# Optimization experiments

Hardware: AMD Instinct MI355X
Metric: run time of the kernel (lower is better)

The kernel has to match this reference:

```python
import jax, jax.numpy as jnp
import numpy as np

HIDDEN = 1024
NUM_HEADS = 4
HEAD_DIM = HIDDEN // NUM_HEADS
SCALE = HEAD_DIM ** -0.5
EPS = 1e-5


def setup_inputs() -> dict:
    key = jax.random.key(0)
    ks = jax.random.split(key, 8)
    B, S, D = 4, 2048, HIDDEN
    x = jax.random.normal(ks[0], (B, S, D), dtype=jnp.float32)
    attention_mask = jnp.ones((B, S), dtype=jnp.int32)
    init = 1.0 / np.sqrt(D)
    Wq = jax.random.uniform(ks[1], (D, D), jnp.float32, -init, init)
    Wk = jax.random.uniform(ks[2], (D, D), jnp.float32, -init, init)
    Wv = jax.random.uniform(ks[3], (D, D), jnp.float32, -init, init)
    Wo = jax.random.uniform(ks[4], (D, D), jnp.float32, -init, init)
    bo = jax.random.uniform(ks[5], (D,), jnp.float32, -init, init)
    gamma = jnp.ones((D,), dtype=jnp.float32)
    beta = jnp.zeros((D,), dtype=jnp.float32)
    return {"x": x, "attention_mask": attention_mask, "Wq": Wq, "Wk": Wk,
            "Wv": Wv, "Wo": Wo, "bo": bo, "gamma": gamma, "beta": beta}


def reference(x, attention_mask, Wq, Wk, Wv, Wo, bo, gamma, beta):
    # Linear layers: y = x @ W^T (torch nn.Linear convention), no bias for q/k/v
    q = jnp.einsum('bsd,ed->bse', x, Wq)
    k = jnp.einsum('bsd,ed->bse', x, Wk)
    v = jnp.einsum('bsd,ed->bse', x, Wv)
    # Full-width attention (module never splits heads), scale = head_dim^-0.5
    scores = jnp.einsum('bqd,bkd->bqk', q, k) * SCALE  # [B,S,S]
    mask = attention_mask[:, None, :]  # [B,1,S]
    scores = jnp.where(mask == 0, jnp.float32(-1e9), scores)
    attn = jax.nn.softmax(scores, axis=-1)
    ctx = jnp.einsum('bqk,bkd->bqd', attn, v)
    out = jnp.einsum('bsd,ed->bse', ctx, Wo) + bo
    # residual + LayerNorm
    h = out + x
    mu = jnp.mean(h, axis=-1, keepdims=True)
    var = jnp.mean(jnp.square(h - mu), axis=-1, keepdims=True)
    return (h - mu) * jax.lax.rsqrt(var + EPS) * gamma + beta
```

## Files before the change

kernel.cpp:

```cpp
#include <hip/hip_runtime.h>

typedef __bf16 bf16;
typedef __bf16 bf16x8 __attribute__((ext_vector_type(8)));
typedef __bf16 bf16x4 __attribute__((ext_vector_type(4)));
typedef float floatx4 __attribute__((ext_vector_type(4)));

#define HIDDEN 1024
#define SEQ 2048
#define BATCH 4
#define ATT_SCALE 0.0625f
#define LN_EPS 1e-5f
#define WW (HIDDEN * HIDDEN)

__device__ __forceinline__ void gload_lds16(const void* g, void* l) {
    __builtin_amdgcn_global_load_lds(
        (const __attribute__((address_space(1))) unsigned int*)g,
        (__attribute__((address_space(3))) unsigned int*)l, 16, 0, 0);
}

#define GBAR() asm volatile("s_barrier" ::: "memory")
#define MFMA(a, b, c) __builtin_amdgcn_mfma_f32_16x16x32_bf16(a, b, c, 0, 0, 0)

__global__ void cvt_f32_bf16(const float* __restrict__ in, bf16* __restrict__ out, int n4) {
    int i = blockIdx.x * blockDim.x + threadIdx.x;
    if (i >= n4) return;
    float4 v = ((const float4*)in)[i];
    bf16x4 o;
    o[0] = (bf16)v.x; o[1] = (bf16)v.y; o[2] = (bf16)v.z; o[3] = (bf16)v.w;
    ((bf16x4*)out)[i] = o;
}

__global__ void transpose_w3(const float* __restrict__ s0, const float* __restrict__ s1,
                             const float* __restrict__ s2,
                             bf16* __restrict__ d0p, bf16* __restrict__ d1p, bf16* __restrict__ d2p) {
    const float* in = (blockIdx.z == 0) ? s0 : (blockIdx.z == 1) ? s1 : s2;
    bf16* out = (blockIdx.z == 0) ? d0p : (blockIdx.z == 1) ? d1p : d2p;
    __shared__ __attribute__((aligned(16))) bf16 tile[64][72];
    const int d0 = blockIdx.x * 64;
    const int f0 = blockIdx.y * 64;
    const int t = threadIdx.x;
    const int r = t >> 4;
    const int c = (t & 15) * 4;
#pragma unroll
    for (int i = 0; i < 4; ++i) {
        float4 v = *(const float4*)&in[(long)(f0 + r + i * 16) * HIDDEN + d0 + c];
        bf16x4 b;
        b[0] = (bf16)v.x; b[1] = (bf16)v.y; b[2] = (bf16)v.z; b[3] = (bf16)v.w;
        *(bf16x4*)&tile[r + i * 16][c] = b;
    }
    __syncthreads();
#pragma unroll
    for (int i = 0; i < 4; ++i) {
        const int dr = r + i * 16;
        bf16x4 o;
#pragma unroll
        for (int j = 0; j < 4; ++j) o[j] = tile[c + j][dr];
        *(bf16x4*)&out[(long)(d0 + dr) * HIDDEN + f0 + c] = o;
    }
}

template <int BNv, int MODE>
__global__ __launch_bounds__(512, 2)
void gemm256(const bf16* A, const bf16* Bw, void* __restrict__ Cout,
             int lda, int ldb, int ldc, int K, float scale,
             long sA, long sB, long sC, int zmod) {
    constexpr int ABY = 256 * 128;
    constexpr int BBY = BNv * 128;
    constexpr int SLOT = ABY + BBY;
    constexpr int AU = ABY / 8192;
    constexpr int BU = BBY / 8192;
    constexpr int WNc = (BNv == 256) ? 4 : 2;
    constexpr int MR = (BNv == 256) ? 8 : 4;
    constexpr int MH = MR / 2;

    __shared__ __attribute__((aligned(16))) char lds[2 * SLOT];

    const int gx = gridDim.x;
    const int nblk = gx * gridDim.y;
    const int bid = blockIdx.y * gx + blockIdx.x;
    const int cpx = nblk >> 3;
    const int sbid = (nblk & 7) ? bid : (bid & 7) * cpx + (bid >> 3);
    const int bx = sbid % gx, by = sbid / gx;

    const int z = blockIdx.z;
    const int mat = z % zmod, ks = z / zmod;
    const char* Ab = (const char*)(A + (long)mat * sA + (long)ks * K);
    const char* Bb = (const char*)(Bw + (long)mat * sB + (long)ks * K);
    const long lda2 = lda * 2L, ldb2 = ldb * 2L;

    const int t = threadIdx.x;
    const int lane = t & 63;
    const int w = t >> 6;
    const int wm = w / WNc, wn = w % WNc;
    const int l15 = lane & 15;
    const int l4 = lane >> 4;

    const int row0 = by * 256;
    const int col0 = bx * BNv;

    const int srow = t >> 3;
    const int soff = (((t & 7) - (srow & 7)) & 7) * 16;
    const char* aP = Ab + (long)(row0 + srow) * lda2 + soff;
    const char* bP = Bb + (long)(col0 + srow) * ldb2 + soff;
    const int ld16 = t * 16;

    auto STAGE = [&](int slot, long koff) {
        char* base = &lds[slot * SLOT];
#pragma unroll
        for (int u = 0; u < AU; ++u)
            gload_lds16(aP + u * 64 * lda2 + koff, base + u * 8192 + ld16);
#pragma unroll
        for (int u = 0; u < BU; ++u)
            gload_lds16(bP + u * 64 * ldb2 + koff, base + ABY + u * 8192 + ld16);
    };

    floatx4 acc[MR][4] = {};
    const int nk = K / 64;

    STAGE(0, 0);
    asm volatile("s_waitcnt vmcnt(0)" ::: "memory");
    GBAR();

    for (int tt = 0; tt < nk; ++tt) {
        const char* sb = &lds[(tt & 1) * SLOT];

        auto RDA = [&](int m, int kkh) {
            int lr = wm * (MR * 16) + m * 16 + l15;
            return *(const bf16x8*)(sb + lr * 128 + (((kkh * 4 + l4 + lr) & 7) << 4));
        };
        auto RDB = [&](int n, int kkh) {
            int lr = wn * 64 + n * 16 + l15;
            return *(const bf16x8*)(sb + ABY + lr * 128 + (((kkh * 4 + l4 + lr) & 7) << 4));
        };

        bf16x8 alo[MH][2], ahi[MH][2], b0[2][2], b1[2][2];
#pragma unroll
        for (int m = 0; m < MH; ++m) { alo[m][0] = RDA(m, 0); alo[m][1] = RDA(m, 1); }
#pragma unroll
        for (int n = 0; n < 2; ++n) {
            b0[n][0] = RDB(n, 0); b0[n][1] = RDB(n, 1);
            b1[n][0] = RDB(2 + n, 0); b1[n][1] = RDB(2 + n, 1);
        }

        if (tt + 1 < nk) STAGE((tt + 1) & 1, (long)(tt + 1) * 128);

        __builtin_amdgcn_s_setprio(1);
#pragma unroll
        for (int m = 0; m < MH; ++m)
#pragma unroll
            for (int n = 0; n < 2; ++n) {
                acc[m][n] = MFMA(alo[m][0], b0[n][0], acc[m][n]);
                acc[m][n] = MFMA(alo[m][1], b0[n][1], acc[m][n]);
            }
        __builtin_amdgcn_s_setprio(0);

#pragma unroll
        for (int m = 0; m < MH; ++m) { ahi[m][0] = RDA(MH + m, 0); ahi[m][1] = RDA(MH + m, 1); }

        __builtin_amdgcn_s_setprio(1);
#pragma unroll
        for (int m = 0; m < MH; ++m)
#pragma unroll
            for (int n = 0; n < 2; ++n) {
                acc[m][2 + n] = MFMA(alo[m][0], b1[n][0], acc[m][2 + n]);
                acc[m][2 + n] = MFMA(alo[m][1], b1[n][1], acc[m][2 + n]);
            }
#pragma unroll
        for (int m = 0; m < MH; ++m)
#pragma unroll
            for (int n = 0; n < 2; ++n) {
                acc[MH + m][n] = MFMA(ahi[m][0], b0[n][0], acc[MH + m][n]);
                acc[MH + m][n] = MFMA(ahi[m][1], b0[n][1], acc[MH + m][n]);
            }
#pragma unroll
        for (int m = 0; m < MH; ++m)
#pragma unroll
            for (int n = 0; n < 2; ++n) {
                acc[MH + m][2 + n] = MFMA(ahi[m][0], b1[n][0], acc[MH + m][2 + n]);
                acc[MH + m][2 + n] = MFMA(ahi[m][1], b1[n][1], acc[MH + m][2 + n]);
            }
        __builtin_amdgcn_s_setprio(0);

        asm volatile("s_waitcnt vmcnt(0)" ::: "memory");
        GBAR();
    }

    const int rq = l4 * 4;
    if constexpr (MODE == 0) {
        bf16* C = ((bf16*)Cout) + (long)z * sC;
#pragma unroll
        for (int m = 0; m < MR; ++m)
#pragma unroll
            for (int i = 0; i < 4; ++i) {
                long gr = row0 + wm * (MR * 16) + m * 16 + rq + i;
#pragma unroll
                for (int n = 0; n < 4; ++n) {
                    int gc = col0 + wn * 64 + n * 16 + l15;
                    C[gr * ldc + gc] = (bf16)(acc[m][n][i] * scale);
                }
            }
    } else {
        float* C = (float*)Cout + (long)z * sC;
#pragma unroll
        for (int m = 0; m < MR; ++m)
#pragma unroll
            for (int i = 0; i < 4; ++i) {
                long gr = row0 + wm * (MR * 16) + m * 16 + rq + i;
#pragma unroll
                for (int n = 0; n < 4; ++n) {
                    int gc = col0 + wn * 64 + n * 16 + l15;
                    C[gr * ldc + gc] = acc[m][n][i];
                }
            }
    }
}

__global__ void reduce_wgc(const float* __restrict__ p, bf16* __restrict__ out) {
    int i = blockIdx.x * blockDim.x + threadIdx.x;
    int e = i * 4;
    int mat = e >> 20;
    int local = e & (WW - 1);
    float4 s = *(const float4*)(p + (long)mat * WW + local);
#pragma unroll
    for (int ksp = 1; ksp < 4; ++ksp) {
        float4 a = *(const float4*)(p + (long)(ksp * 2 + mat) * WW + local);
        s.x += a.x; s.y += a.y; s.z += a.z; s.w += a.w;
    }
    bf16x4 o;
    o[0] = (bf16)s.x; o[1] = (bf16)s.y; o[2] = (bf16)s.z; o[3] = (bf16)s.w;
    *(bf16x4*)&out[e] = o;
}

__global__ void softmax_rows(bf16* __restrict__ S, const int* __restrict__ mask) {
    const int b = blockIdx.y;
    const int row = blockIdx.x;
    bf16* srow = S + ((long)b * SEQ + row) * SEQ;
    const int* mrow = mask + b * SEQ;
    const int t = threadIdx.x;

    bf16x8 sv = *(const bf16x8*)&srow[t * 8];
    int4 m0 = ((const int4*)mrow)[t * 2];
    int4 m1 = ((const int4*)mrow)[t * 2 + 1];
    int mk[8] = {m0.x, m0.y, m0.z, m0.w, m1.x, m1.y, m1.z, m1.w};

    float v[8];
    float mx = -1e30f;
#pragma unroll
    for (int j = 0; j < 8; ++j) {
        float s = (float)sv[j];
        if (mk[j] == 0) s = -1e9f;
        v[j] = s;
        mx = fmaxf(mx, s);
    }
    __shared__ float redm[4], reds[4];
#pragma unroll
    for (int off = 32; off > 0; off >>= 1) mx = fmaxf(mx, __shfl_down(mx, off));
    if ((t & 63) == 0) redm[t >> 6] = mx;
    __syncthreads();
    mx = fmaxf(fmaxf(redm[0], redm[1]), fmaxf(redm[2], redm[3]));

    float sum = 0.f;
#pragma unroll
    for (int j = 0; j < 8; ++j) {
        v[j] = __expf(v[j] - mx);
        sum += v[j];
    }
#pragma unroll
    for (int off = 32; off > 0; off >>= 1) sum += __shfl_down(sum, off);
    if ((t & 63) == 0) reds[t >> 6] = sum;
    __syncthreads();
    sum = reds[0] + reds[1] + reds[2] + reds[3];
    float inv = 1.0f / sum;

    bf16x8 o;
#pragma unroll
    for (int j = 0; j < 8; ++j) o[j] = (bf16)(v[j] * inv);
    *(bf16x8*)&srow[t * 8] = o;
}

__global__ void transpose_v(const bf16* __restrict__ yv, bf16* __restrict__ out) {
    __shared__ __attribute__((aligned(16))) bf16 tile[64][72];
    const int z = blockIdx.z;
    const bf16* ib = yv + (long)z * SEQ * 2048 + 1024;
    bf16* ob = out + (long)z * SEQ * HIDDEN;
    const int d0 = blockIdx.x * 64;
    const int s0 = blockIdx.y * 64;
    const int t = threadIdx.x;
    const int r = t >> 4;
    const int c = (t & 15) * 4;
#pragma unroll
    for (int i = 0; i < 4; ++i) {
        bf16x4 v = *(const bf16x4*)&ib[(long)(s0 + r + i * 16) * 2048 + d0 + c];
        *(bf16x4*)&tile[r + i * 16][c] = v;
    }
    __syncthreads();
#pragma unroll
    for (int i = 0; i < 4; ++i) {
        const int dr = r + i * 16;
        bf16x4 o;
#pragma unroll
        for (int j = 0; j < 4; ++j) o[j] = tile[c + j][dr];
        *(bf16x4*)&ob[(long)(d0 + dr) * SEQ + s0 + c] = o;
    }
}

__global__ void layernorm_out(const bf16* __restrict__ pp, const float* __restrict__ x,
                              const float* __restrict__ bo, const float* __restrict__ gamma,
                              const float* __restrict__ beta, float* __restrict__ out) {
    const long row = blockIdx.x;
    const int b = (int)(row >> 11);
    const int s = (int)(row & 2047);
    const bf16* r0 = pp + ((long)b * SEQ + s) * HIDDEN;
    const bf16* r1 = r0 + 4L * SEQ * HIDDEN;
    const int t = threadIdx.x;

    bf16x4 a0 = ((const bf16x4*)r0)[t];
    bf16x4 a1 = ((const bf16x4*)r1)[t];
    float4 xv = ((const float4*)(x + row * HIDDEN))[t];
    float4 bv = ((const float4*)bo)[t];
    float4 v;
    v.x = (float)a0[0] + (float)a1[0] + bv.x + xv.x;
    v.y = (float)a0[1] + (float)a1[1] + bv.y + xv.y;
    v.z = (float)a0[2] + (float)a1[2] + bv.z + xv.z;
    v.w = (float)a0[3] + (float)a1[3] + bv.w + xv.w;

    float ssum = v.x + v.y + v.z + v.w;
    float sq = v.x * v.x + v.y * v.y + v.z * v.z + v.w * v.w;
    __shared__ float rs[4], rq[4];
#pragma unroll
    for (int off = 32; off > 0; off >>= 1) {
        ssum += __shfl_down(ssum, off);
        sq += __shfl_down(sq, off);
    }
    if ((t & 63) == 0) { rs[t >> 6] = ssum; rq[t >> 6] = sq; }
    __syncthreads();
    ssum = rs[0] + rs[1] + rs[2] + rs[3];
    sq = rq[0] + rq[1] + rq[2] + rq[3];
    float mu = ssum * (1.0f / HIDDEN);
    float var = sq * (1.0f / HIDDEN) - mu * mu;
    float rinv = rsqrtf(var + LN_EPS);
    float4 g = ((const float4*)gamma)[t];
    float4 bt = ((const float4*)beta)[t];
    float4 o;
    o.x = (v.x - mu) * rinv * g.x + bt.x;
    o.y = (v.y - mu) * rinv * g.y + bt.y;
    o.z = (v.z - mu) * rinv * g.z + bt.z;
    o.w = (v.w - mu) * rinv * g.w + bt.w;
    ((float4*)(out + row * HIDDEN))[t] = o;
}

extern "C" void kernel_launch(void* const* d_in, const int* in_sizes, int n_in,
                              void* d_out, int out_size, void* d_ws, size_t ws_size,
                              hipStream_t stream) {
    const float* x     = (const float*)d_in[0];
    const int*   mask  = (const int*)d_in[1];
    const float* Wq    = (const float*)d_in[2];
    const float* Wk    = (const float*)d_in[3];
    const float* Wv    = (const float*)d_in[4];
    const float* Wo    = (const float*)d_in[5];
    const float* bo    = (const float*)d_in[6];
    const float* gamma = (const float*)d_in[7];
    const float* beta  = (const float*)d_in[8];
    float* out = (float*)d_out;

    char* ws = (char*)d_ws;
    const long MB = 1024L * 1024L;
    bf16* yv   = (bf16*)(ws + 0 * MB);
    bf16* pp   = (bf16*)(ws + 0 * MB);
    bf16* xb   = (bf16*)(ws + 32 * MB);
    bf16* vt   = (bf16*)(ws + 48 * MB);
    bf16* wgc  = (bf16*)(ws + 64 * MB);
    bf16* wkT  = (bf16*)(ws + 68 * MB);
    bf16* wo   = (bf16*)(ws + 70 * MB);
    bf16* wqT  = (bf16*)(ws + 72 * MB);
    bf16* wvT  = (bf16*)(ws + 74 * MB);
    bf16* S    = (bf16*)(ws + 76 * MB);
    float* wgcp = (float*)(ws + 76 * MB);

    const int BS = BATCH * SEQ;
    dim3 blk256(256), blk512(512);

    cvt_f32_bf16<<<dim3(BS * HIDDEN / 4 / 256), blk256, 0, stream>>>(x, xb, BS * HIDDEN / 4);
    cvt_f32_bf16<<<dim3(WW / 4 / 256), blk256, 0, stream>>>(Wo, wo, WW / 4);
    transpose_w3<<<dim3(16, 16, 3), blk256, 0, stream>>>(Wq, Wk, Wv, wqT, wkT, wvT);

    gemm256<128, 4><<<dim3(HIDDEN / 128, HIDDEN / 256, 8), blk512, 0, stream>>>(
        wkT, wqT, wgcp, HIDDEN, HIDDEN, HIDDEN, 256, 1.0f,
        (long)WW, (long)WW, (long)WW, 2);
    reduce_wgc<<<dim3(2 * WW / 4 / 256), blk256, 0, stream>>>(wgcp, wgc);

    gemm256<256, 0><<<dim3(2048 / 256, BS / 256, 1), blk512, 0, stream>>>(
        xb, wgc, yv, HIDDEN, HIDDEN, 2048, HIDDEN, 1.0f, 0, 0, 0, 1);

    transpose_v<<<dim3(HIDDEN / 64, SEQ / 64, BATCH), blk256, 0, stream>>>(yv, vt);

    gemm256<256, 0><<<dim3(SEQ / 256, SEQ / 256, BATCH), blk512, 0, stream>>>(
        yv, xb, S, 2048, HIDDEN, SEQ, HIDDEN, ATT_SCALE,
        (long)SEQ * 2048, (long)SEQ * HIDDEN, (long)SEQ * SEQ, 4);

    softmax_rows<<<dim3(SEQ, BATCH), blk256, 0, stream>>>(S, mask);

    gemm256<128, 0><<<dim3(HIDDEN / 128, SEQ / 256, 8), blk512, 0, stream>>>(
        S, vt, pp, SEQ, SEQ, HIDDEN, 1024, 1.0f,
        (long)SEQ * SEQ, (long)HIDDEN * SEQ, (long)SEQ * HIDDEN, 4);

    layernorm_out<<<dim3(BS), blk256, 0, stream>>>(pp, x, bo, gamma, beta, out);
}
```

Before: 187.9 us.

## Replace GEMM with 8-phase pipelined 256x256 kernel using split-K LDS slots

Replaces the templated GEMM with a single 256x256-tile kernel that splits each 64-wide K step into two 32-wide halves stored as separate A/B LDS sub-buffers. Loads for the next tile are issued in four stages interleaved with four MFMA phases, each bracketed by barriers and partial vmcnt waits. The goal is to overlap global-to-LDS traffic with compute and to avoid draining all loads at every iteration. The two GEMMs that used 128-wide tiles now also use 256x256 tiles, which halves their block count. The extra barriers add synchronisation cost, and the fewer blocks may leave CUs underused on the smaller GEMMs.

After: 186.8 us. Within noise of the previous version (-0.6%).

```diff
diff --git a/kernel.cpp b/kernel.cpp
--- a/kernel.cpp
+++ b/kernel.cpp
@@ -19,6 +19,9 @@
 }
 
 #define GBAR() asm volatile("s_barrier" ::: "memory")
+#define LGKM0() do { asm volatile("s_waitcnt lgkmcnt(0)" ::: "memory"); \
+                     __builtin_amdgcn_sched_barrier(0); } while (0)
+#define VMC(N) asm volatile("s_waitcnt vmcnt(" #N ")" ::: "memory")
 #define MFMA(a, b, c) __builtin_amdgcn_mfma_f32_16x16x32_bf16(a, b, c, 0, 0, 0)
 
 __global__ void cvt_f32_bf16(const float* __restrict__ in, bf16* __restrict__ out, int n4) {
@@ -59,21 +62,12 @@
     }
 }
 
-template <int BNv, int MODE>
+template <int MODE>
 __global__ __launch_bounds__(512, 2)
-void gemm256(const bf16* A, const bf16* Bw, void* __restrict__ Cout,
-             int lda, int ldb, int ldc, int K, float scale,
-             long sA, long sB, long sC, int zmod) {
-    constexpr int ABY = 256 * 128;
-    constexpr int BBY = BNv * 128;
-    constexpr int SLOT = ABY + BBY;
-    constexpr int AU = ABY / 8192;
-    constexpr int BU = BBY / 8192;
-    constexpr int WNc = (BNv == 256) ? 4 : 2;
-    constexpr int MR = (BNv == 256) ? 8 : 4;
-    constexpr int MH = MR / 2;
-
-    __shared__ __attribute__((aligned(16))) char lds[2 * SLOT];
+void gemm8p(const bf16* A, const bf16* Bw, void* __restrict__ Cout,
+            int lda, int ldb, int ldc, int K, float scale,
+            long sA, long sB, long sC, int zmod) {
+    __shared__ __attribute__((aligned(16))) char lds[131072];
 
     const int gx = gridDim.x;
     const int nblk = gx * gridDim.y;
@@ -91,108 +85,122 @@
     const int t = threadIdx.x;
     const int lane = t & 63;
     const int w = t >> 6;
-    const int wm = w / WNc, wn = w % WNc;
+    const int wm = w >> 2;
+    const int wn = w & 3;
     const int l15 = lane & 15;
     const int l4 = lane >> 4;
 
     const int row0 = by * 256;
-    const int col0 = bx * BNv;
-
-    const int srow = t >> 3;
-    const int soff = (((t & 7) - (srow & 7)) & 7) * 16;
-    const char* aP = Ab + (long)(row0 + srow) * lda2 + soff;
-    const char* bP = Bb + (long)(col0 + srow) * ldb2 + soff;
-    const int ld16 = t * 16;
-
-    auto STAGE = [&](int slot, long koff) {
-        char* base = &lds[slot * SLOT];
-#pragma unroll
-        for (int u = 0; u < AU; ++u)
-            gload_lds16(aP + u * 64 * lda2 + koff, base + u * 8192 + ld16);
-#pragma unroll
-        for (int u = 0; u < BU; ++u)
-            gload_lds16(bP + u * 64 * ldb2 + koff, base + ABY + u * 8192 + ld16);
+    const int col0 = bx * 256;
+
+    const int sc = ((((t & 3) - ((t >> 3) & 3)) & 3) << 4);
+    const char* aS[2];
+    const char* bS[2];
+#pragma unroll
+    for (int uu = 0; uu < 2; ++uu) {
+        aS[uu] = Ab + (long)(row0 + uu * 128 + (t >> 2)) * lda2 + sc;
+        bS[uu] = Bb + (long)(col0 + uu * 128 + (t >> 2)) * ldb2 + sc;
+    }
+
+    auto STAGE = [&](char* dstu, const char* const* sp, long koff) {
+        gload_lds16(sp[0] + koff, dstu + t * 16);
+        gload_lds16(sp[1] + koff, dstu + 8192 + t * 16);
     };
 
-    floatx4 acc[MR][4] = {};
+    floatx4 acc[8][4] = {};
     const int nk = K / 64;
 
-    STAGE(0, 0);
-    asm volatile("s_waitcnt vmcnt(0)" ::: "memory");
+    STAGE(lds + 0,     aS, 0);
+    STAGE(lds + 16384, bS, 0);
+    STAGE(lds + 32768, aS, 64);
+    STAGE(lds + 49152, bS, 64);
+    VMC(4);
     GBAR();
 
     for (int tt = 0; tt < nk; ++tt) {
-        const char* sb = &lds[(tt & 1) * SLOT];
-
-        auto RDA = [&](int m, int kkh) {
-            int lr = wm * (MR * 16) + m * 16 + l15;
-            return *(const bf16x8*)(sb + lr * 128 + (((kkh * 4 + l4 + lr) & 7) << 4));
+        const char* cb = lds + (tt & 1) * 65536;
+        char* nb = lds + ((tt & 1) ^ 1) * 65536;
+        const long nko = (long)((tt + 1 < nk) ? tt + 1 : nk - 1) * 128;
+
+        auto RDA = [&](int kk, int m) {
+            int lr = wm * 128 + m * 16 + l15;
+            return *(const bf16x8*)(cb + kk * 32768 + lr * 64 + ((((lr >> 1) + l4) & 3) << 4));
         };
-        auto RDB = [&](int n, int kkh) {
+        auto RDB = [&](int kk, int n) {
             int lr = wn * 64 + n * 16 + l15;
-            return *(const bf16x8*)(sb + ABY + lr * 128 + (((kkh * 4 + l4 + lr) & 7) << 4));
+            return *(const bf16x8*)(cb + 16384 + kk * 32768 + lr * 64 + ((((lr >> 1) + l4) & 3) << 4));
         };
 
-        bf16x8 alo[MH][2], ahi[MH][2], b0[2][2], b1[2][2];
-#pragma unroll
-        for (int m = 0; m < MH; ++m) { alo[m][0] = RDA(m, 0); alo[m][1] = RDA(m, 1); }
-#pragma unroll
-        for (int n = 0; n < 2; ++n) {
-            b0[n][0] = RDB(n, 0); b0[n][1] = RDB(n, 1);
-            b1[n][0] = RDB(2 + n, 0); b1[n][1] = RDB(2 + n, 1);
-        }
-
-        if (tt + 1 < nk) STAGE((tt + 1) & 1, (long)(tt + 1) * 128);
-
+        bf16x8 a[4], b0[4], b1[4];
+
+#pragma unroll
+        for (int m = 0; m < 4; ++m) a[m] = RDA(0, m);
+#pragma unroll
+        for (int n = 0; n < 4; ++n) b0[n] = RDB(0, n);
+        STAGE(nb + 0, aS, nko);
+        GBAR();
+        LGKM0();
         __builtin_amdgcn_s_setprio(1);
 #pragma unroll
-        for (int m = 0; m < MH; ++m)
-#pragma unroll
-            for (int n = 0; n < 2; ++n) {
-                acc[m][n] = MFMA(alo[m][0], b0[n][0], acc[m][n]);
-                acc[m][n] = MFMA(alo[m][1], b0[n][1], acc[m][n]);
-            }
+        for (int m = 0; m < 4; ++m)
+#pragma unroll
+            for (int n = 0; n < 4; ++n) acc[m][n] = MFMA(a[m], b0[n], acc[m][n]);
         __builtin_amdgcn_s_setprio(0);
-
-#pragma unroll
-        for (int m = 0; m < MH; ++m) { ahi[m][0] = RDA(MH + m, 0); ahi[m][1] = RDA(MH + m, 1); }
-
+        GBAR();
+
+#pragma unroll
+        for (int m = 0; m < 4; ++m) a[m] = RDA(0, 4 + m);
+        STAGE(nb + 16384, bS, nko);
+        GBAR();
+        LGKM0();
         __builtin_amdgcn_s_setprio(1);
 #pragma unroll
-        for (int m = 0; m < MH; ++m)
-#pragma unroll
-            for (int n = 0; n < 2; ++n) {
-                acc[m][2 + n] = MFMA(alo[m][0], b1[n][0], acc[m][2 + n]);
-                acc[m][2 + n] = MFMA(alo[m][1], b1[n][1], acc[m][2 + n]);
-            }
-#pragma unroll
-        for (int m = 0; m < MH; ++m)
-#pragma unroll
-            for (int n = 0; n < 2; ++n) {
-                acc[MH + m][n] = MFMA(ahi[m][0], b0[n][0], acc[MH + m][n]);
-                acc[MH + m][n] = MFMA(ahi[m][1], b0[n][1], acc[MH + m][n]);
-            }
-#pragma unroll
-        for (int m = 0; m < MH; ++m)
-#pragma unroll
-            for (int n = 0; n < 2; ++n) {
-                acc[MH + m][2 + n] = MFMA(ahi[m][0], b1[n][0], acc[MH + m][2 + n]);
-                acc[MH + m][2 + n] = MFMA(ahi[m][1], b1[n][1], acc[MH + m][2 + n]);
-            }
+        for (int m = 0; m < 4; ++m)
+#pragma unroll
+            for (int n = 0; n < 4; ++n) acc[4 + m][n] = MFMA(a[m], b0[n], acc[4 + m][n]);
         __builtin_amdgcn_s_setprio(0);
-
-        asm volatile("s_waitcnt vmcnt(0)" ::: "memory");
-        GBAR();
-    }
+        VMC(4);
+        GBAR();
+
+#pragma unroll
+        for (int m = 0; m < 4; ++m) a[m] = RDA(1, m);
+#pragma unroll
+        for (int n = 0; n < 4; ++n) b1[n] = RDB(1, n);
+        STAGE(nb + 32768, aS, nko + 64);
+        GBAR();
+        LGKM0();
+        __builtin_amdgcn_s_setprio(1);
+#pragma unroll
+        for (int m = 0; m < 4; ++m)
+#pragma unroll
+            for (int n = 0; n < 4; ++n) acc[m][n] = MFMA(a[m], b1[n], acc[m][n]);
+        __builtin_amdgcn_s_setprio(0);
+        GBAR();
+
+#pragma unroll
+        for (int m = 0; m < 4; ++m) a[m] = RDA(1, 4 + m);
+        STAGE(nb + 49152, bS, nko + 64);
+        GBAR();
+        LGKM0();
+        __builtin_amdgcn_s_setprio(1);
+#pragma unroll
+        for (int m = 0; m < 4; ++m)
+#pragma unroll
+            for (int n = 0; n < 4; ++n) acc[4 + m][n] = MFMA(a[m], b1[n], acc[4 + m][n]);
+        __builtin_amdgcn_s_setprio(0);
+        VMC(4);
+        GBAR();
+    }
+    VMC(0);
 
     const int rq = l4 * 4;
     if constexpr (MODE == 0) {
         bf16* C = ((bf16*)Cout) + (long)z * sC;
 #pragma unroll
-        for (int m = 0; m < MR; ++m)
+        for (int m = 0; m < 8; ++m)
 #pragma unroll
             for (int i = 0; i < 4; ++i) {
-                long gr = row0 + wm * (MR * 16) + m * 16 + rq + i;
+                long gr = row0 + wm * 128 + m * 16 + rq + i;
 #pragma unroll
                 for (int n = 0; n < 4; ++n) {
                     int gc = col0 + wn * 64 + n * 16 + l15;
@@ -202,10 +210,10 @@
     } else {
         float* C = (float*)Cout + (long)z * sC;
 #pragma unroll
-        for (int m = 0; m < MR; ++m)
+        for (int m = 0; m < 8; ++m)
 #pragma unroll
             for (int i = 0; i < 4; ++i) {
-                long gr = row0 + wm * (MR * 16) + m * 16 + rq + i;
+                long gr = row0 + wm * 128 + m * 16 + rq + i;
 #pragma unroll
                 for (int n = 0; n < 4; ++n) {
                     int gc = col0 + wn * 64 + n * 16 + l15;
@@ -384,23 +392,23 @@
     cvt_f32_bf16<<<dim3(WW / 4 / 256), blk256, 0, stream>>>(Wo, wo, WW / 4);
     transpose_w3<<<dim3(16, 16, 3), blk256, 0, stream>>>(Wq, Wk, Wv, wqT, wkT, wvT);
 
-    gemm256<128, 4><<<dim3(HIDDEN / 128, HIDDEN / 256, 8), blk512, 0, stream>>>(
+    gemm8p<4><<<dim3(1024 / 256, 1024 / 256, 8), blk512, 0, stream>>>(
         wkT, wqT, wgcp, HIDDEN, HIDDEN, HIDDEN, 256, 1.0f,
         (long)WW, (long)WW, (long)WW, 2);
     reduce_wgc<<<dim3(2 * WW / 4 / 256), blk256, 0, stream>>>(wgcp, wgc);
 
-    gemm256<256, 0><<<dim3(2048 / 256, BS / 256, 1), blk512, 0, stream>>>(
+    gemm8p<0><<<dim3(2048 / 256, BS / 256, 1), blk512, 0, stream>>>(
         xb, wgc, yv, HIDDEN, HIDDEN, 2048, HIDDEN, 1.0f, 0, 0, 0, 1);
 
     transpose_v<<<dim3(HIDDEN / 64, SEQ / 64, BATCH), blk256, 0, stream>>>(yv, vt);
 
-    gemm256<256, 0><<<dim3(SEQ / 256, SEQ / 256, BATCH), blk512, 0, stream>>>(
+    gemm8p<0><<<dim3(SEQ / 256, SEQ / 256, BATCH), blk512, 0, stream>>>(
         yv, xb, S, 2048, HIDDEN, SEQ, HIDDEN, ATT_SCALE,
         (long)SEQ * 2048, (long)SEQ * HIDDEN, (long)SEQ * SEQ, 4);
 
     softmax_rows<<<dim3(SEQ, BATCH), blk256, 0, stream>>>(S, mask);
 
-    gemm256<128, 0><<<dim3(HIDDEN / 128, SEQ / 256, 8), blk512, 0, stream>>>(
+    gemm8p<0><<<dim3(HIDDEN / 256, SEQ / 256, 8), blk512, 0, stream>>>(
         S, vt, pp, SEQ, SEQ, HIDDEN, 1024, 1.0f,
         (long)SEQ * SEQ, (long)HIDDEN * SEQ, (long)SEQ * HIDDEN, 4);
 
```
